# Kernel optimization log

Measured on AMD Instinct MI355X. Metric: run time of the kernel, lower is better.

The kernel has to match this reference:

```python
import jax, jax.numpy as jnp
from jax import lax
import numpy as np

NUM_KIND = 4
V, H, B = 34, 32, 4096   # raw vertical (2 rows dropped), horizontal, batch
KS = 33                  # odd-rounded max(V-2, H)
NUM_DEPTH = 4
N_SQ = 100


def _conv(x, w):
    # x: (N,1,h,w), w: (1,1,KS,KS); torch Conv2d == cross-correlation == lax default
    return lax.conv_general_dilated(x, w, (1, 1), 'SAME',
                                    dimension_numbers=('NCHW', 'OIHW', 'NCHW'))


def _conv_k(x, w):
    # x: (K,B,1,h,w) -> conv each map with the shared 1-channel kernel
    k, b, c, h, wd = x.shape
    return _conv(x.reshape(k * b, c, h, wd), w).reshape(k, b, c, h, wd)


def setup_inputs() -> dict:
    key = jax.random.key(0)
    ks = jax.random.split(key, 8)
    std = 0.3
    return {
        'dots':    jax.random.randint(ks[0], (V, H, B), 0, NUM_KIND + 1, dtype=jnp.int32),
        'w_each':  jax.random.normal(ks[1], (1, 1, KS, KS), jnp.float32) * std,
        'w_not':   jax.random.normal(ks[2], (1, 1, KS, KS), jnp.float32) * std,
        'w_not2':  jax.random.normal(ks[3], (1, 1, KS, KS), jnp.float32) * std,
        'w_empty': jax.random.normal(ks[4], (1, 1, KS, KS), jnp.float32) * std,
        'W1':      jax.random.normal(ks[5], (N_SQ, (V - 2) * H), jnp.float32) * std,
        'W2':      jax.random.normal(ks[6], (N_SQ, N_SQ), jnp.float32) * std,
        'W3':      jax.random.normal(ks[7], (1, N_SQ), jnp.float32) * std,
    }


def reference(dots, w_each, w_not, w_not2, w_empty, W1, W2, W3):
    # drop last 2 vertical rows, layout (V-2,H,B) -> (B,1,V-2,H)
    board = dots[:-2].astype(jnp.float32).transpose(2, 0, 1)[:, None]  # (B,1,h,w)

    empty = (board == 0).astype(jnp.float32)
    E = _conv(empty, w_empty)                                           # (B,1,h,w)

    kinds = jnp.arange(1, NUM_KIND + 1, dtype=board.dtype).reshape(NUM_KIND, 1, 1, 1, 1)
    each = (board[None] == kinds).astype(jnp.float32)                   # (K,B,1,h,w)
    notm = ((each + empty[None]) == 0).astype(jnp.float32)              # (K,B,1,h,w)

    # first pass: per-color value, masked to that color's cells
    notm_conv = _conv_k(notm, w_not)      # note: the torch code LOGS the convolved not-mask
    v = _conv_k(each, w_each) + E[None] - notm_conv
    L = each * v                          # each_color_value_log (masked)
    s = jax.nn.sigmoid(L.sum(axis=0))     # all_color_value_2nd, (B,1,h,w)

    # iterative diffusion; torch mutates the log in-place each depth:
    # L <- mask * (L + E + conv2nd(notm_conv * before)); before is detached
    for _ in range(NUM_DEPTH):
        before = lax.stop_gradient(s)
        C = _conv_k(notm_conv * before[None], w_not2)
        L = each * (L + E[None] + C)
        s = jax.nn.sigmoid(L.sum(axis=0))

    feat = s.reshape(s.shape[0], -1)      # (B, (V-2)*H)
    x = jax.nn.leaky_relu(feat @ W1.T, 0.2)
    x = jax.nn.leaky_relu(x @ W2.T, 0.2)
    return x @ W3.T                        # (B,1)
```

## Files before the change

### kernel.cpp

```cpp
#include <hip/hip_runtime.h>
#include <cstdint>
#include <cstddef>


typedef _Float16 f16;
typedef __attribute__((ext_vector_type(8))) _Float16 f16x8;
typedef __attribute__((ext_vector_type(4))) float f32x4;

#define NB   4096
#define PIX  1024
#define MR   (NB * 4)

__device__ __forceinline__ void gld_lds16(const void* g, void* l) {
    __builtin_amdgcn_global_load_lds(
        (const __attribute__((address_space(1))) void*)g,
        (__attribute__((address_space(3))) void*)l, 16, 0, 0);
}

__device__ __forceinline__ void band_range(int otile, int& t_lo, int& t_hi) {
    int i0 = otile >> 5;
    t_lo = (i0 > 16) ? ((i0 - 16) >> 1) : 0;
    t_hi = (i0 + 19) >> 1;
    if (t_hi > 15) t_hi = 15;
}

__global__ void build_all(const float* __restrict__ we, const float* __restrict__ wn,
                          const float* __restrict__ wn2, const float* __restrict__ wem,
                          const float* __restrict__ W1, const int* __restrict__ dots,
                          f16* __restrict__ Me, f16* __restrict__ Mn,
                          f16* __restrict__ Mn2, f16* __restrict__ Mem,
                          f16* __restrict__ W1b, unsigned char* __restrict__ board,
                          f16* __restrict__ eachF, f16* __restrict__ notmF,
                          f16* __restrict__ emptyF) {
    __shared__ unsigned char tile[64][68];
    int bi = blockIdx.x, t = threadIdx.x;
    if (bi < 4096) {
        int idx = bi * 256 + t;
        int o = idx >> 10, in = idx & 1023;
        int i = o >> 5, j = o & 31, a = in >> 5, b = in & 31;
        int u = a - i + 16, v = b - j + 16;
        bool ok = (u >= 0) && (u < 33) && (v >= 0) && (v < 33);
        int w = u * 33 + v;
        float ve = 0.f, vn = 0.f, vn2 = 0.f, vem = 0.f;
        if (ok) { ve = we[w]; vn = wn[w]; vn2 = wn2[w]; vem = wem[w]; }
        Me[idx]  = (f16)ve;
        Mn[idx]  = (f16)vn;
        Mn2[idx] = (f16)vn2;
        Mem[idx] = (f16)vem;
    } else if (bi < 4608) {
        int idx = (bi - 4096) * 256 + t;
        int j = idx >> 10, i = idx & 1023;
        W1b[idx] = (f16)(j < 100 ? W1[j * 1024 + i] : 0.f);
    } else {
        int bb = bi - 4608;
        int bp = bb & 15, bn = bb >> 4;
        int p0 = bp * 64, n0 = bn * 64;
        int ln = t & 63, lp = t >> 6;
#pragma unroll
        for (int j = 0; j < 16; j++) {
            int p = lp * 16 + j;
            tile[p][ln] = (unsigned char)dots[(size_t)(p0 + p) * 4096 + n0 + ln];
        }
        __syncthreads();
#pragma unroll
        for (int j = 0; j < 16; j++) {
            int n = lp * 16 + j;
            unsigned char c = tile[ln][n];
            size_t nrow = (size_t)(n0 + n);
            board[nrow * 1024 + p0 + ln] = c;
            emptyF[nrow * PIX + p0 + ln] = (c == 0) ? (f16)1.f : (f16)0.f;
            size_t r0 = (nrow * 4) * PIX + p0 + ln;
#pragma unroll
            for (int k = 0; k < 4; k++) {
                unsigned char k1 = (unsigned char)(k + 1);
                eachF[r0 + (size_t)k * PIX] = (c == k1) ? (f16)1.f : (f16)0.f;
                notmF[r0 + (size_t)k * PIX] =
                    (c != 0 && c != k1) ? (f16)1.f : (f16)0.f;
            }
        }
    }
}

template <int MODE>
__device__ __forceinline__ void run_gemm(
    int bjob, int ypx, int nx, char* smem,
    const f16* __restrict__ X, const f16* __restrict__ B,
    const unsigned char* __restrict__ board, const f16* __restrict__ En,
    const f16* __restrict__ NCs, f16* __restrict__ Lsel,
    f16* __restrict__ Pout, f16* __restrict__ outB, int ldo) {
    char* smB = smem;
    char* smA = smem + 16384;

    const int tid = threadIdx.x;
    const int wv = tid >> 6, ln = tid & 63;
    const int wm = wv >> 1, wn_ = wv & 1;
    const int lr = ln & 15, lq = ln >> 4;

    int xcd = bjob & 7, slot = bjob >> 3;
    int bx = slot % nx;
    int by = xcd * ypx + slot / nx;
    const int rtile = by * 128, otile = bx * 128;

    int t_lo, t_hi;
    band_range(otile, t_lo, t_hi);

    const f32x4 fz = {0.f, 0.f, 0.f, 0.f};
    f32x4 acc[4][4];
#pragma unroll
    for (int i = 0; i < 4; i++)
#pragma unroll
        for (int j = 0; j < 4; j++) acc[i][j] = fz;

    for (int kt = t_lo; kt <= t_hi; kt++) {
        const int kb = kt * 64;
#pragma unroll
        for (int t = 0; t < 4; t++) {
            int c = (wv * 4 + t) * 64 + ln;
            int row = c >> 3, gcol = (c & 7) ^ (row & 7);
            gld_lds16(B + (size_t)(otile + row) * 1024 + kb + gcol * 8, smB + c * 16);
            gld_lds16(X + (size_t)(rtile + row) * 1024 + kb + gcol * 8, smA + c * 16);
        }
        __syncthreads();

#pragma unroll
        for (int kk = 0; kk < 2; kk++) {
            const int oct = kk * 4 + lq;
            f16x8 af[4], bfr[4];
#pragma unroll
            for (int i = 0; i < 4; i++) {
                int rrow = wm * 64 + i * 16 + lr;
                af[i] = *(const f16x8*)(smA + rrow * 128 + (oct ^ (rrow & 7)) * 16);
            }
#pragma unroll
            for (int j = 0; j < 4; j++) {
                int brow = wn_ * 64 + j * 16 + lr;
                bfr[j] = *(const f16x8*)(smB + brow * 128 + (oct ^ (brow & 7)) * 16);
            }
#pragma unroll
            for (int i = 0; i < 4; i++)
#pragma unroll
                for (int j = 0; j < 4; j++)
                    acc[i][j] = __builtin_amdgcn_mfma_f32_16x16x32_f16(
                        af[i], bfr[j], acc[i][j], 0, 0, 0);
        }
        __syncthreads();
    }

    if constexpr (MODE == 0) {
        f16* sT = (f16*)smem;
#pragma unroll
        for (int i = 0; i < 4; i++) {
            int rb = wm * 64 + i * 16 + lq * 4;
#pragma unroll
            for (int j = 0; j < 4; j++) {
                int col = wn_ * 64 + j * 16 + lr;
                f32x4 a = acc[i][j];
#pragma unroll
                for (int v = 0; v < 4; v++)
                    sT[(rb + v) * 136 + col] = (f16)a[v];
            }
        }
        __syncthreads();
#pragma unroll
        for (int it = 0; it < 8; it++) {
            int row = it * 16 + (tid >> 4), cg = tid & 15;
            f16x8 vv = *(const f16x8*)(sT + row * 136 + cg * 8);
            *(f16x8*)(outB + (size_t)(rtile + row) * ldo + otile + cg * 8) = vv;
        }
    } else {
        float* sAcc = (float*)smem;
#pragma unroll
        for (int h = 0; h < 2; h++) {
            if (wm == h) {
#pragma unroll
                for (int i = 0; i < 4; i++) {
                    int lrow = i * 16 + lq * 4;
#pragma unroll
                    for (int j = 0; j < 4; j++) {
                        int col = wn_ * 64 + j * 16 + lr;
                        f32x4 a = acc[i][j];
#pragma unroll
                        for (int v = 0; v < 4; v++)
                            sAcc[(lrow + v) * 132 + col] = a[v];
                    }
                }
            }
            __syncthreads();
            {
                int cell = tid >> 4, cg = tid & 15;
                int rb = rtile + h * 64 + cell * 4;
                int ngl = rb >> 2;
                int o = otile + cg * 8;
                size_t no = (size_t)ngl * PIX + o;
                uint64_t bb = *(const uint64_t*)(board + no);
                f16x8 en8 = *(const f16x8*)(En + no);
                size_t r0 = (size_t)rb * PIX + o;
                f16x8 nc0 = *(const f16x8*)(NCs + r0);
                f16x8 nc1 = *(const f16x8*)(NCs + r0 + PIX);
                f16x8 nc2 = *(const f16x8*)(NCs + r0 + 2 * PIX);
                f16x8 nc3 = *(const f16x8*)(NCs + r0 + 3 * PIX);
                const float* ar = sAcc + cell * 4 * 132 + cg * 8;
                f32x4 arow[4][2];
#pragma unroll
                for (int k = 0; k < 4; k++) {
                    arow[k][0] = *(const f32x4*)(ar + k * 132);
                    arow[k][1] = *(const f32x4*)(ar + k * 132 + 4);
                }
                f16x8 lout, p0, p1, p2, p3;
#pragma unroll
                for (int j2 = 0; j2 < 8; j2++) {
                    int c = (int)((bb >> (8 * j2)) & 0xff);
                    float a0 = arow[0][j2 >> 2][j2 & 3];
                    float a1 = arow[1][j2 >> 2][j2 & 3];
                    float a2 = arow[2][j2 >> 2][j2 & 3];
                    float a3 = arow[3][j2 >> 2][j2 & 3];
                    float asel = (c == 1) ? a0 : (c == 2) ? a1 : (c == 3) ? a2 : a3;
                    float L = 0.f;
                    if (c > 0) {
                        float ncsel = (float)((c == 1) ? nc0[j2] : (c == 2) ? nc1[j2]
                                            : (c == 3) ? nc2[j2] : nc3[j2]);
                        L = asel + (float)en8[j2] - ncsel;
                    }
                    lout[j2] = (f16)L;
                    f16 s = (f16)(1.f / (1.f + __expf(-L)));
                    p0[j2] = nc0[j2] * s;
                    p1[j2] = nc1[j2] * s;
                    p2[j2] = nc2[j2] * s;
                    p3[j2] = nc3[j2] * s;
                }
                *(f16x8*)(Lsel + no)            = lout;
                *(f16x8*)(Pout + r0)            = p0;
                *(f16x8*)(Pout + r0 + PIX)      = p1;
                *(f16x8*)(Pout + r0 + 2 * PIX)  = p2;
                *(f16x8*)(Pout + r0 + 3 * PIX)  = p3;
            }
            __syncthreads();
        }
    }
}

__global__ void __launch_bounds__(256, 4) gemm_faA(
    const f16* __restrict__ Mn, const f16* __restrict__ Mem,
    const f16* __restrict__ notmF, const f16* __restrict__ emptyF,
    f16* __restrict__ NC, f16* __restrict__ En) {
    __shared__ __attribute__((aligned(16))) char smem[34816];
    int bi = blockIdx.x;
    if (bi < 1024) {
        run_gemm<0>(bi, 16, 8, smem, notmF, Mn, nullptr, nullptr, nullptr,
                    nullptr, nullptr, NC, PIX);
    } else {
        run_gemm<0>(bi - 1024, 4, 8, smem, emptyF, Mem, nullptr, nullptr, nullptr,
                    nullptr, nullptr, En, PIX);
    }
}

__global__ void __launch_bounds__(256, 4) gemm_faB(
    const f16* __restrict__ Me, const f16* __restrict__ eachF,
    const unsigned char* __restrict__ board, const f16* __restrict__ En,
    const f16* __restrict__ NC, f16* __restrict__ Lsel, f16* __restrict__ P1) {
    __shared__ __attribute__((aligned(16))) char smem[36864];
    run_gemm<2>(blockIdx.x, 16, 8, smem, eachF, Me, board, En, NC,
                Lsel, P1, nullptr, 0);
}

template <int MODE>
__global__ void __launch_bounds__(256, 4) gemm_depth(
    const f16* __restrict__ Pin, const f16* __restrict__ Mn2,
    const unsigned char* __restrict__ board, const f16* __restrict__ NC,
    const f16* __restrict__ En, f16* __restrict__ Lsel,
    f16* __restrict__ Pout, f16* __restrict__ feat) {
    __shared__ __attribute__((aligned(16))) char smem[36864];
    char* smB = smem;
    char* smA = smem + 16384;

    const int tid = threadIdx.x;
    const int wv = tid >> 6, ln = tid & 63;
    const int wm = wv >> 1, wn_ = wv & 1;
    const int lr = ln & 15, lq = ln >> 4;

    int bi = blockIdx.x;
    int xcd = bi & 7, slot = bi >> 3;
    int bx = slot & 7;
    int by = xcd * 16 + (slot >> 3);
    const int rtile = by * 128, otile = bx * 128;

    int t_lo, t_hi;
    band_range(otile, t_lo, t_hi);

    const f32x4 fz = {0.f, 0.f, 0.f, 0.f};
    f32x4 acc[4][4];
#pragma unroll
    for (int i = 0; i < 4; i++)
#pragma unroll
        for (int j = 0; j < 4; j++) acc[i][j] = fz;

    for (int kt = t_lo; kt <= t_hi; kt++) {
        const int kb = kt * 64;
#pragma unroll
        for (int t = 0; t < 4; t++) {
            int c = (wv * 4 + t) * 64 + ln;
            int row = c >> 3, gcol = (c & 7) ^ (row & 7);
            gld_lds16(Mn2 + (size_t)(otile + row) * 1024 + kb + gcol * 8, smB + c * 16);
            gld_lds16(Pin + (size_t)(rtile + row) * 1024 + kb + gcol * 8, smA + c * 16);
        }
        __syncthreads();

#pragma unroll
        for (int kk = 0; kk < 2; kk++) {
            const int oct = kk * 4 + lq;
            f16x8 af[4], bfr[4];
#pragma unroll
            for (int i = 0; i < 4; i++) {
                int rrow = wm * 64 + i * 16 + lr;
                af[i] = *(const f16x8*)(smA + rrow * 128 + (oct ^ (rrow & 7)) * 16);
            }
#pragma unroll
            for (int j = 0; j < 4; j++) {
                int brow = wn_ * 64 + j * 16 + lr;
                bfr[j] = *(const f16x8*)(smB + brow * 128 + (oct ^ (brow & 7)) * 16);
            }
#pragma unroll
            for (int i = 0; i < 4; i++)
#pragma unroll
                for (int j = 0; j < 4; j++)
                    acc[i][j] = __builtin_amdgcn_mfma_f32_16x16x32_f16(
                        af[i], bfr[j], acc[i][j], 0, 0, 0);
        }
        __syncthreads();
    }

    float* sAcc = (float*)smem;
#pragma unroll
    for (int h = 0; h < 2; h++) {
        if (wm == h) {
#pragma unroll
            for (int i = 0; i < 4; i++) {
                int lrow = i * 16 + lq * 4;
#pragma unroll
                for (int j = 0; j < 4; j++) {
                    int col = wn_ * 64 + j * 16 + lr;
                    f32x4 a = acc[i][j];
#pragma unroll
                    for (int v = 0; v < 4; v++)
                        sAcc[(lrow + v) * 132 + col] = a[v];
                }
            }
        }
        __syncthreads();
        {
            int cell = tid >> 4, cg = tid & 15;
            int rb = rtile + h * 64 + cell * 4;
            int ngl = rb >> 2;
            int o = otile + cg * 8;
            size_t no = (size_t)ngl * PIX + o;
            uint64_t bb = *(const uint64_t*)(board + no);
            f16x8 en8 = *(const f16x8*)(En + no);
            f16x8 ls8 = *(const f16x8*)(Lsel + no);
            const float* ar = sAcc + cell * 4 * 132 + cg * 8;
            f32x4 arow[4][2];
#pragma unroll
            for (int k = 0; k < 4; k++) {
                arow[k][0] = *(const f32x4*)(ar + k * 132);
                arow[k][1] = *(const f32x4*)(ar + k * 132 + 4);
            }
            if constexpr (MODE == 4) {
                f16x8 s8;
#pragma unroll
                for (int j2 = 0; j2 < 8; j2++) {
                    int c = (int)((bb >> (8 * j2)) & 0xff);
                    float a0 = arow[0][j2 >> 2][j2 & 3];
                    float a1 = arow[1][j2 >> 2][j2 & 3];
                    float a2 = arow[2][j2 >> 2][j2 & 3];
                    float a3 = arow[3][j2 >> 2][j2 & 3];
                    float asel = (c == 1) ? a0 : (c == 2) ? a1 : (c == 3) ? a2 : a3;
                    float L = 0.f;
                    if (c > 0) L = (float)ls8[j2] + (float)en8[j2] + asel;
                    s8[j2] = (f16)(1.f / (1.f + __expf(-L)));
                }
                *(f16x8*)(feat + no) = s8;
            } else {
                size_t r0 = (size_t)rb * PIX + o;
                f16x8 nc0 = *(const f16x8*)(NC + r0);
                f16x8 nc1 = *(const f16x8*)(NC + r0 + PIX);
                f16x8 nc2 = *(const f16x8*)(NC + r0 + 2 * PIX);
                f16x8 nc3 = *(const f16x8*)(NC + r0 + 3 * PIX);
                f16x8 lout, p0, p1, p2, p3;
#pragma unroll
                for (int j2 = 0; j2 < 8; j2++) {
                    int c = (int)((bb >> (8 * j2)) & 0xff);
                    float a0 = arow[0][j2 >> 2][j2 & 3];
                    float a1 = arow[1][j2 >> 2][j2 & 3];
                    float a2 = arow[2][j2 >> 2][j2 & 3];
                    float a3 = arow[3][j2 >> 2][j2 & 3];
                    float asel = (c == 1) ? a0 : (c == 2) ? a1 : (c == 3) ? a2 : a3;
                    float L = 0.f;
                    if (c > 0) L = (float)ls8[j2] + (float)en8[j2] + asel;
                    lout[j2] = (f16)L;
                    f16 s = (f16)(1.f / (1.f + __expf(-L)));
                    p0[j2] = nc0[j2] * s;
                    p1[j2] = nc1[j2] * s;
                    p2[j2] = nc2[j2] * s;
                    p3[j2] = nc3[j2] * s;
                }
                *(f16x8*)(Lsel + no)           = lout;
                *(f16x8*)(Pout + r0)           = p0;
                *(f16x8*)(Pout + r0 + PIX)     = p1;
                *(f16x8*)(Pout + r0 + 2 * PIX) = p2;
                *(f16x8*)(Pout + r0 + 3 * PIX) = p3;
            }
        }
        __syncthreads();
    }
}

__global__ void __launch_bounds__(256) gemm_mlp_fused(
    const f16* __restrict__ feat, const f16* __restrict__ W1b,
    const float* __restrict__ W2, const float* __restrict__ W3,
    float* __restrict__ out) {
    __shared__ __attribute__((aligned(16))) char smem[47360];
    char* smB = smem;
    char* smA = smem + 16384;

    const int tid = threadIdx.x;
    const int wv = tid >> 6, ln = tid & 63;
    const int wm = wv >> 1, wn_ = wv & 1;
    const int lr = ln & 15, lq = ln >> 4;
    const int rtile = blockIdx.x * 64;

    const f32x4 fz = {0.f, 0.f, 0.f, 0.f};
    f32x4 acc[2][4];
#pragma unroll
    for (int i = 0; i < 2; i++)
#pragma unroll
        for (int j = 0; j < 4; j++) acc[i][j] = fz;

    for (int kb = 0; kb < 1024; kb += 64) {
#pragma unroll
        for (int t = 0; t < 4; t++) {
            int c = (wv * 4 + t) * 64 + ln;
            int row = c >> 3, gcol = (c & 7) ^ (row & 7);
            gld_lds16(W1b + (size_t)row * 1024 + kb + gcol * 8, smB + c * 16);
        }
#pragma unroll
        for (int t = 0; t < 2; t++) {
            int c = t * 256 + tid;
            int row = c >> 3, gcol = (c & 7) ^ (row & 7);
            gld_lds16(feat + (size_t)(rtile + row) * 1024 + kb + gcol * 8, smA + c * 16);
        }
        __syncthreads();
#pragma unroll
        for (int kk = 0; kk < 2; kk++) {
            const int oct = kk * 4 + lq;
            f16x8 af[2], bfr[4];
#pragma unroll
            for (int i = 0; i < 2; i++) {
                int rrow = wm * 32 + i * 16 + lr;
                af[i] = *(const f16x8*)(smA + rrow * 128 + (oct ^ (rrow & 7)) * 16);
            }
#pragma unroll
            for (int j = 0; j < 4; j++) {
                int brow = wn_ * 64 + j * 16 + lr;
                bfr[j] = *(const f16x8*)(smB + brow * 128 + (oct ^ (brow & 7)) * 16);
            }
#pragma unroll
            for (int i = 0; i < 2; i++)
#pragma unroll
                for (int j = 0; j < 4; j++)
                    acc[i][j] = __builtin_amdgcn_mfma_f32_16x16x32_f16(
                        af[i], bfr[j], acc[i][j], 0, 0, 0);
        }
        __syncthreads();
    }

    float* xs  = (float*)smem;
    f16*   sW2 = (f16*)(smem + 25856);
    float* sW3 = (float*)(smem + 45856);
    float* red = (float*)(smem + 46272);
    for (int idx = tid; idx < 10000; idx += 256) sW2[idx] = (f16)W2[idx];
    if (tid < 100) sW3[tid] = W3[tid];

#pragma unroll
    for (int i = 0; i < 2; i++) {
        int rb = wm * 32 + i * 16 + lq * 4;
#pragma unroll
        for (int j = 0; j < 4; j++) {
            int o = wn_ * 64 + j * 16 + lr;
            if (o < 100) {
                f32x4 a = acc[i][j];
#pragma unroll
                for (int v = 0; v < 4; v++) {
                    float x = a[v];
                    xs[(rb + v) * 101 + o] = x > 0.f ? x : 0.2f * x;
                }
            }
        }
    }
    __syncthreads();
    {
        int nb = tid >> 2, q = tid & 3;
        const float* xrow = xs + nb * 101;
        float partial = 0.f;
        for (int jj = 0; jj < 25; jj++) {
            int j = q + jj * 4;
            const f16* w2r = sW2 + j * 100;
            float a2 = 0.f;
#pragma unroll
            for (int i = 0; i < 100; i++) a2 += (float)w2r[i] * xrow[i];
            partial += sW3[j] * (a2 > 0.f ? a2 : 0.2f * a2);
        }
        red[tid] = partial;
        __syncthreads();
        if (q == 0)
            out[rtile + nb] = red[tid] + red[tid + 1] + red[tid + 2] + red[tid + 3];
    }
}

extern "C" void kernel_launch(void* const* d_in, const int* in_sizes, int n_in,
                              void* d_out, int out_size, void* d_ws, size_t ws_size,
                              hipStream_t stream) {
    (void)in_sizes; (void)n_in; (void)out_size; (void)ws_size;
    const int*   dots   = (const int*)d_in[0];
    const float* w_each = (const float*)d_in[1];
    const float* w_not  = (const float*)d_in[2];
    const float* w_not2 = (const float*)d_in[3];
    const float* w_emp  = (const float*)d_in[4];
    const float* W1 = (const float*)d_in[5];
    const float* W2 = (const float*)d_in[6];
    const float* W3 = (const float*)d_in[7];
    float* out = (float*)d_out;

    char* ws = (char*)d_ws;
    size_t off = 0;
    auto alloc = [&](size_t bytes) -> char* {
        char* p = ws + off;
        off += (bytes + 255) & ~(size_t)255;
        return p;
    };
    f16* Me    = (f16*)alloc((size_t)PIX * PIX * 2);
    f16* Mn    = (f16*)alloc((size_t)PIX * PIX * 2);
    f16* Mn2   = (f16*)alloc((size_t)PIX * PIX * 2);
    f16* Mem   = (f16*)alloc((size_t)PIX * PIX * 2);
    f16* W1b   = (f16*)alloc((size_t)128 * PIX * 2);
    unsigned char* board = (unsigned char*)alloc((size_t)NB * PIX);
    f16* eachF = (f16*)alloc((size_t)MR * PIX * 2);
    f16* notmF = (f16*)alloc((size_t)MR * PIX * 2);
    f16* emptyF= (f16*)alloc((size_t)NB * PIX * 2);
    f16* NC    = (f16*)alloc((size_t)MR * PIX * 2);
    f16* En    = (f16*)alloc((size_t)NB * PIX * 2);
    f16* Lsel  = (f16*)alloc((size_t)NB * PIX * 2);
    f16* feat  = (f16*)alloc((size_t)NB * PIX * 2);
    f16* Pa = notmF;
    f16* Pb = eachF;

    dim3 blk(256);
    build_all<<<5632, blk, 0, stream>>>(w_each, w_not, w_not2, w_emp, W1, dots,
                                        Me, Mn, Mn2, Mem, W1b, board,
                                        eachF, notmF, emptyF);
    gemm_faA<<<1280, blk, 0, stream>>>(Mn, Mem, notmF, emptyF, NC, En);
    gemm_faB<<<1024, blk, 0, stream>>>(Me, eachF, board, En, NC, Lsel, Pa);
    gemm_depth<3><<<1024, blk, 0, stream>>>(Pa, Mn2, board, NC, En, Lsel, Pb, nullptr);
    gemm_depth<3><<<1024, blk, 0, stream>>>(Pb, Mn2, board, NC, En, Lsel, Pa, nullptr);
    gemm_depth<3><<<1024, blk, 0, stream>>>(Pa, Mn2, board, NC, En, Lsel, Pb, nullptr);
    gemm_depth<4><<<1024, blk, 0, stream>>>(Pb, Mn2, board, NC, En, Lsel, nullptr, feat);
    gemm_mlp_fused<<<64, blk, 0, stream>>>(feat, W1b, W2, W3, out);
}
```

Before: 364.7 us.

## Balance band-tile scheduling, prefetch epilogue operands, and split MLP into more blocks

Column tiles are remapped so alternating groups of slots walk the banded output tiles in reverse order, spreading heavy and light K-ranges across CUs. The epilogue's global loads of board, En, Lsel and NC are issued before the LDS accumulator staging and barrier, so their latency overlaps the shared-memory writes. The fused MLP kernel now uses 32-row tiles across 128 blocks instead of 64-row tiles across 64, with 8 threads per row in the W2 stage, to fill more CUs. The trade-offs are higher register pressure from holding prefetched vectors and W2/W3 being reloaded into LDS by twice as many blocks.

```diff
diff --git a/kernel.cpp b/kernel.cpp
--- a/kernel.cpp
+++ b/kernel.cpp
@@ -22,6 +22,11 @@
     t_lo = (i0 > 16) ? ((i0 - 16) >> 1) : 0;
     t_hi = (i0 + 19) >> 1;
     if (t_hi > 15) t_hi = 15;
+}
+
+__device__ __forceinline__ int bx_balanced(int slot, int nx) {
+    int base = slot % nx;
+    return ((slot >> 5) & 1) ? (nx - 1 - base) : base;
 }
 
 __global__ void build_all(const float* __restrict__ we, const float* __restrict__ wn,
@@ -97,7 +102,7 @@
     const int lr = ln & 15, lq = ln >> 4;
 
     int xcd = bjob & 7, slot = bjob >> 3;
-    int bx = slot % nx;
+    int bx = bx_balanced(slot, nx);
     int by = xcd * ypx + slot / nx;
     const int rtile = by * 128, otile = bx * 128;
 
@@ -171,6 +176,18 @@
         float* sAcc = (float*)smem;
 #pragma unroll
         for (int h = 0; h < 2; h++) {
+            int cell = tid >> 4, cg = tid & 15;
+            int rb = rtile + h * 64 + cell * 4;
+            int ngl = rb >> 2;
+            int o = otile + cg * 8;
+            size_t no = (size_t)ngl * PIX + o;
+            size_t r0 = (size_t)rb * PIX + o;
+            uint64_t bb = *(const uint64_t*)(board + no);
+            f16x8 en8 = *(const f16x8*)(En + no);
+            f16x8 nc0 = *(const f16x8*)(NCs + r0);
+            f16x8 nc1 = *(const f16x8*)(NCs + r0 + PIX);
+            f16x8 nc2 = *(const f16x8*)(NCs + r0 + 2 * PIX);
+            f16x8 nc3 = *(const f16x8*)(NCs + r0 + 3 * PIX);
             if (wm == h) {
 #pragma unroll
                 for (int i = 0; i < 4; i++) {
@@ -187,18 +204,6 @@
             }
             __syncthreads();
             {
-                int cell = tid >> 4, cg = tid & 15;
-                int rb = rtile + h * 64 + cell * 4;
-                int ngl = rb >> 2;
-                int o = otile + cg * 8;
-                size_t no = (size_t)ngl * PIX + o;
-                uint64_t bb = *(const uint64_t*)(board + no);
-                f16x8 en8 = *(const f16x8*)(En + no);
-                size_t r0 = (size_t)rb * PIX + o;
-                f16x8 nc0 = *(const f16x8*)(NCs + r0);
-                f16x8 nc1 = *(const f16x8*)(NCs + r0 + PIX);
-                f16x8 nc2 = *(const f16x8*)(NCs + r0 + 2 * PIX);
-                f16x8 nc3 = *(const f16x8*)(NCs + r0 + 3 * PIX);
                 const float* ar = sAcc + cell * 4 * 132 + cg * 8;
                 f32x4 arow[4][2];
 #pragma unroll
@@ -280,7 +285,7 @@
 
     int bi = blockIdx.x;
     int xcd = bi & 7, slot = bi >> 3;
-    int bx = slot & 7;
+    int bx = bx_balanced(slot, 8);
     int by = xcd * 16 + (slot >> 3);
     const int rtile = by * 128, otile = bx * 128;
 
@@ -332,6 +337,22 @@
     float* sAcc = (float*)smem;
 #pragma unroll
     for (int h = 0; h < 2; h++) {
+        int cell = tid >> 4, cg = tid & 15;
+        int rb = rtile + h * 64 + cell * 4;
+        int ngl = rb >> 2;
+        int o = otile + cg * 8;
+        size_t no = (size_t)ngl * PIX + o;
+        size_t r0 = (size_t)rb * PIX + o;
+        uint64_t bb = *(const uint64_t*)(board + no);
+        f16x8 en8 = *(const f16x8*)(En + no);
+        f16x8 ls8 = *(const f16x8*)(Lsel + no);
+        f16x8 nc0, nc1, nc2, nc3;
+        if constexpr (MODE == 3) {
+            nc0 = *(const f16x8*)(NC + r0);
+            nc1 = *(const f16x8*)(NC + r0 + PIX);
+            nc2 = *(const f16x8*)(NC + r0 + 2 * PIX);
+            nc3 = *(const f16x8*)(NC + r0 + 3 * PIX);
+        }
         if (wm == h) {
 #pragma unroll
             for (int i = 0; i < 4; i++) {
@@ -348,14 +369,6 @@
         }
         __syncthreads();
         {
-            int cell = tid >> 4, cg = tid & 15;
-            int rb = rtile + h * 64 + cell * 4;
-            int ngl = rb >> 2;
-            int o = otile + cg * 8;
-            size_t no = (size_t)ngl * PIX + o;
-            uint64_t bb = *(const uint64_t*)(board + no);
-            f16x8 en8 = *(const f16x8*)(En + no);
-            f16x8 ls8 = *(const f16x8*)(Lsel + no);
             const float* ar = sAcc + cell * 4 * 132 + cg * 8;
             f32x4 arow[4][2];
 #pragma unroll
@@ -379,11 +392,6 @@
                 }
                 *(f16x8*)(feat + no) = s8;
             } else {
-                size_t r0 = (size_t)rb * PIX + o;
-                f16x8 nc0 = *(const f16x8*)(NC + r0);
-                f16x8 nc1 = *(const f16x8*)(NC + r0 + PIX);
-                f16x8 nc2 = *(const f16x8*)(NC + r0 + 2 * PIX);
-                f16x8 nc3 = *(const f16x8*)(NC + r0 + 3 * PIX);
                 f16x8 lout, p0, p1, p2, p3;
 #pragma unroll
                 for (int j2 = 0; j2 < 8; j2++) {
@@ -425,14 +433,12 @@
     const int wv = tid >> 6, ln = tid & 63;
     const int wm = wv >> 1, wn_ = wv & 1;
     const int lr = ln & 15, lq = ln >> 4;
-    const int rtile = blockIdx.x * 64;
+    const int rtile = blockIdx.x * 32;
 
     const f32x4 fz = {0.f, 0.f, 0.f, 0.f};
-    f32x4 acc[2][4];
-#pragma unroll
-    for (int i = 0; i < 2; i++)
-#pragma unroll
-        for (int j = 0; j < 4; j++) acc[i][j] = fz;
+    f32x4 acc[4];
+#pragma unroll
+    for (int j = 0; j < 4; j++) acc[j] = fz;
 
     for (int kb = 0; kb < 1024; kb += 64) {
 #pragma unroll
@@ -441,33 +447,27 @@
             int row = c >> 3, gcol = (c & 7) ^ (row & 7);
             gld_lds16(W1b + (size_t)row * 1024 + kb + gcol * 8, smB + c * 16);
         }
-#pragma unroll
-        for (int t = 0; t < 2; t++) {
-            int c = t * 256 + tid;
-            int row = c >> 3, gcol = (c & 7) ^ (row & 7);
-            gld_lds16(feat + (size_t)(rtile + row) * 1024 + kb + gcol * 8, smA + c * 16);
+        {
+            int row = tid >> 3, gcol = (tid & 7) ^ (row & 7);
+            gld_lds16(feat + (size_t)(rtile + row) * 1024 + kb + gcol * 8,
+                      smA + tid * 16);
         }
         __syncthreads();
 #pragma unroll
         for (int kk = 0; kk < 2; kk++) {
             const int oct = kk * 4 + lq;
-            f16x8 af[2], bfr[4];
-#pragma unroll
-            for (int i = 0; i < 2; i++) {
-                int rrow = wm * 32 + i * 16 + lr;
-                af[i] = *(const f16x8*)(smA + rrow * 128 + (oct ^ (rrow & 7)) * 16);
-            }
+            int rrow = wm * 16 + lr;
+            f16x8 af = *(const f16x8*)(smA + rrow * 128 + (oct ^ (rrow & 7)) * 16);
+            f16x8 bfr[4];
 #pragma unroll
             for (int j = 0; j < 4; j++) {
                 int brow = wn_ * 64 + j * 16 + lr;
                 bfr[j] = *(const f16x8*)(smB + brow * 128 + (oct ^ (brow & 7)) * 16);
             }
 #pragma unroll
-            for (int i = 0; i < 2; i++)
-#pragma unroll
-                for (int j = 0; j < 4; j++)
-                    acc[i][j] = __builtin_amdgcn_mfma_f32_16x16x32_f16(
-                        af[i], bfr[j], acc[i][j], 0, 0, 0);
+            for (int j = 0; j < 4; j++)
+                acc[j] = __builtin_amdgcn_mfma_f32_16x16x32_f16(
+                    af, bfr[j], acc[j], 0, 0, 0);
         }
         __syncthreads();
     }
@@ -479,14 +479,13 @@
     for (int idx = tid; idx < 10000; idx += 256) sW2[idx] = (f16)W2[idx];
     if (tid < 100) sW3[tid] = W3[tid];
 
-#pragma unroll
-    for (int i = 0; i < 2; i++) {
-        int rb = wm * 32 + i * 16 + lq * 4;
+    {
+        int rb = wm * 16 + lq * 4;
 #pragma unroll
         for (int j = 0; j < 4; j++) {
             int o = wn_ * 64 + j * 16 + lr;
             if (o < 100) {
-                f32x4 a = acc[i][j];
+                f32x4 a = acc[j];
 #pragma unroll
                 for (int v = 0; v < 4; v++) {
                     float x = a[v];
@@ -497,21 +496,27 @@
     }
     __syncthreads();
     {
-        int nb = tid >> 2, q = tid & 3;
+        int nb = tid >> 3, q = tid & 7;
         const float* xrow = xs + nb * 101;
         float partial = 0.f;
-        for (int jj = 0; jj < 25; jj++) {
-            int j = q + jj * 4;
-            const f16* w2r = sW2 + j * 100;
-            float a2 = 0.f;
-#pragma unroll
-            for (int i = 0; i < 100; i++) a2 += (float)w2r[i] * xrow[i];
-            partial += sW3[j] * (a2 > 0.f ? a2 : 0.2f * a2);
+        for (int jj = 0; jj < 13; jj++) {
+            int j = q + jj * 8;
+            if (j < 100) {
+                const f16* w2r = sW2 + j * 100;
+                float a2 = 0.f;
+#pragma unroll
+                for (int i = 0; i < 100; i++) a2 += (float)w2r[i] * xrow[i];
+                partial += sW3[j] * (a2 > 0.f ? a2 : 0.2f * a2);
+            }
         }
         red[tid] = partial;
         __syncthreads();
-        if (q == 0)
-            out[rtile + nb] = red[tid] + red[tid + 1] + red[tid + 2] + red[tid + 3];
+        if (q == 0) {
+            float s = 0.f;
+#pragma unroll
+            for (int k = 0; k < 8; k++) s += red[tid + k];
+            out[rtile + nb] = s;
+        }
     }
 }
 
@@ -562,5 +567,5 @@
     gemm_depth<3><<<1024, blk, 0, stream>>>(Pb, Mn2, board, NC, En, Lsel, Pa, nullptr);
     gemm_depth<3><<<1024, blk, 0, stream>>>(Pa, Mn2, board, NC, En, Lsel, Pb, nullptr);
     gemm_depth<4><<<1024, blk, 0, stream>>>(Pb, Mn2, board, NC, En, Lsel, nullptr, feat);
-    gemm_mlp_fused<<<64, blk, 0, stream>>>(feat, W1b, W2, W3, out);
-}
+    gemm_mlp_fused<<<128, blk, 0, stream>>>(feat, W1b, W2, W3, out);
+}
```

Result: no change. 370.8 us (+1.7%).
